# Kernel tuning notes

Measured on AMD Instinct MI355X. Metric: run time of the kernel, lower is better.

## Reference

```python
import jax, jax.numpy as jnp
import numpy as np

B, T, C = 4, 1024, 1024
H, KV, D = 16, 8, 64   # n_head, kv_heads, dim_head
L = 32                 # partial rotary dim (freqs.shape[-1])
QK_NORM_SCALE = 10.0


def l2norm(t):
    # F.normalize(t, dim=-1): divide by L2 norm clamped to eps
    n = jnp.linalg.norm(t, axis=-1, keepdims=True)
    return t / jnp.maximum(n, 1e-12)


def rotate_half(x):
    # lucidrains rotary: interleaved pairs (d r) with r=2 -> (-x2, x1)
    x1, x2 = x[..., 0::2], x[..., 1::2]
    return jnp.stack((-x2, x1), axis=-1).reshape(x.shape)


def apply_rope(t, freqs):
    # xpos_scale is None in this config -> scale = 1.0
    return t * jnp.cos(freqs) + rotate_half(t) * jnp.sin(freqs)


def setup_inputs() -> dict:
    key = jax.random.key(0)
    ks = jax.random.split(key, 10)
    x = jax.random.normal(ks[0], (B, T, C), dtype=jnp.float32)
    encoded_data = jax.random.normal(ks[1], (B, T, C), dtype=jnp.float32)
    # rotary freqs: positions x inverse frequencies, duplicated interleaved to length L
    pos = jnp.arange(T, dtype=jnp.float32)
    inv_freq = 10000.0 ** (-jnp.arange(L // 2, dtype=jnp.float32) / (L // 2))
    freqs = jnp.repeat(pos[:, None] * inv_freq[None, :], 2, axis=-1)  # (T, L)
    attn_bias = jax.random.normal(ks[2], (H, T, T), dtype=jnp.float32) * 0.02
    Wq = jax.random.normal(ks[3], (C, H * D), dtype=jnp.float32) * 0.02
    Wk = jax.random.normal(ks[4], (C, KV * D), dtype=jnp.float32) * 0.02
    Wv = jax.random.normal(ks[5], (C, KV * D), dtype=jnp.float32) * 0.02
    Wo = jax.random.normal(ks[6], (H * D, C), dtype=jnp.float32) * 0.02
    q_scale = jnp.ones((D,), dtype=jnp.float32)
    k_scale = jnp.ones((D,), dtype=jnp.float32)
    return {"x": x, "encoded_data": encoded_data, "freqs": freqs,
            "attn_bias": attn_bias, "Wq": Wq, "Wk": Wk, "Wv": Wv, "Wo": Wo,
            "q_scale": q_scale, "k_scale": k_scale}


def reference(x, encoded_data, freqs, attn_bias, Wq, Wk, Wv, Wo, q_scale, k_scale):
    Bx, Tx, Cx = x.shape
    q = (x @ Wq).reshape(Bx, Tx, H, D).transpose(0, 2, 1, 3)            # (B,H,T,D)
    k = (encoded_data @ Wk).reshape(Bx, Tx, KV, D).transpose(0, 2, 1, 3)  # (B,KV,T,D)
    v = (encoded_data @ Wv).reshape(Bx, Tx, KV, D).transpose(0, 2, 1, 3)

    # qk-norm
    q = l2norm(q) * q_scale
    k = l2norm(k) * k_scale

    # partial rotary on first L dims (v too, as in the original code)
    l = freqs.shape[-1]
    ql, qr = q[..., :l], q[..., l:]
    kl, kr = k[..., :l], k[..., l:]
    vl, vr = v[..., :l], v[..., l:]
    q = jnp.concatenate([apply_rope(ql, freqs), qr], axis=-1)
    k = jnp.concatenate([apply_rope(kl, freqs), kr], axis=-1)
    v = jnp.concatenate([apply_rope(vl, freqs), vr], axis=-1)

    # GQA: k,v repeated along head dim (KV -> H = 2*KV)
    k = jnp.tile(k, (1, 2, 1, 1))
    v = jnp.tile(v, (1, 2, 1, 1))

    # pre-scale q, then SDPA applies its own default D^-0.5 (faithful to source)
    default_scale = D ** (-0.5)
    q = q * (default_scale / QK_NORM_SCALE)

    mask_value = -jnp.finfo(q.dtype).max
    causal = jnp.triu(jnp.ones((Tx, Tx), dtype=bool), k=1)  # j > i masked
    bias = jnp.where(causal, mask_value / 2, attn_bias)      # (H,T,T)

    scores = jnp.einsum('bhqd,bhkd->bhqk', q, k) * default_scale + bias[None]
    attn = jax.nn.softmax(scores, axis=-1)
    y = jnp.einsum('bhqk,bhkd->bhqd', attn, v)                # (B,H,T,D)
    y = y.transpose(0, 2, 1, 3).reshape(Bx, Tx, H * D)
    return y @ Wo
```

## Files before the change

kernel.cpp:

```cpp
#include <hip/hip_runtime.h>

typedef unsigned short u16;
typedef __attribute__((ext_vector_type(8))) __bf16 bf16x8;
typedef __attribute__((ext_vector_type(4))) float f32x4;
typedef __attribute__((ext_vector_type(16))) float f32x16;

#define LOG2E 1.44269504088896f

__device__ __forceinline__ u16 f2bf(float f) {
  union { float f; unsigned u; } c; c.f = f;
  unsigned u = c.u;
  return (u16)((u + 0x7fffu + ((u >> 16) & 1u)) >> 16);
}
__device__ __forceinline__ float bf2f(u16 h) {
  union { unsigned u; float f; } c; c.u = ((unsigned)h) << 16;
  return c.f;
}

__device__ __forceinline__ void load_lds16(const void* g, void* l) {
  __builtin_amdgcn_global_load_lds((const __attribute__((address_space(1))) unsigned int*)g,
                                   (__attribute__((address_space(3))) unsigned int*)l, 16, 0, 0);
}

__global__ void cast2_kernel(const float* __restrict__ a, const float* __restrict__ b,
                             u16* __restrict__ oa, u16* __restrict__ ob, int n4each) {
  int stride = gridDim.x * blockDim.x;
  for (int i = blockIdx.x * blockDim.x + threadIdx.x; i < 2 * n4each; i += stride) {
    const float4* src; ushort4* dst; int j;
    if (i < n4each) { src = (const float4*)a; dst = (ushort4*)oa; j = i; }
    else            { src = (const float4*)b; dst = (ushort4*)ob; j = i - n4each; }
    float4 v = src[j];
    ushort4 o;
    o.x = f2bf(v.x); o.y = f2bf(v.y); o.z = f2bf(v.z); o.w = f2bf(v.w);
    dst[j] = o;
  }
}

__global__ void trig_kernel(const float* __restrict__ freqs, float* __restrict__ cstab,
                            float* __restrict__ sntab) {
  int i = blockIdx.x * 256 + threadIdx.x;
  float f = freqs[i];
  float sn, cs;
  sincosf(f, &sn, &cs);
  cstab[i] = cs; sntab[i] = sn;
}

__global__ void bias_tiles_kernel(const float* __restrict__ bias, u16* __restrict__ biasTT) {
  int w = threadIdx.x >> 6, lane = threadIdx.x & 63;
  int f = blockIdx.x * 4 + w;
  int h = f / 528, rem = f - h * 528;
  int qt = (int)((sqrtf(8.f * (float)rem + 1.f) - 1.f) * 0.5f);
  while ((qt + 1) * (qt + 2) / 2 <= rem) ++qt;
  while (qt * (qt + 1) / 2 > rem) --qt;
  int kt = rem - qt * (qt + 1) / 2;
  int ql = lane & 31, hi = lane >> 5;
  const float* src = bias + ((size_t)h * 1024 + qt * 32 + ql) * 1024 + kt * 32 + hi * 4;
  u16 v[16];
#pragma unroll
  for (int g2 = 0; g2 < 4; ++g2) {
    float4 c = *(const float4*)(src + g2 * 8);
    v[g2 * 4 + 0] = f2bf(c.x * LOG2E);
    v[g2 * 4 + 1] = f2bf(c.y * LOG2E);
    v[g2 * 4 + 2] = f2bf(c.z * LOG2E);
    v[g2 * 4 + 3] = f2bf(c.w * LOG2E);
  }
  u16* dst = biasTT + (size_t)f * 1024 + lane * 16;
#pragma unroll
  for (int i = 0; i < 4; ++i) {
    ushort4 o; o.x = v[i * 4]; o.y = v[i * 4 + 1]; o.z = v[i * 4 + 2]; o.w = v[i * 4 + 3];
    *(ushort4*)(dst + i * 4) = o;
  }
}

__global__ void transpose_cast4_kernel(const float* __restrict__ Wq, const float* __restrict__ Wk,
                                       const float* __restrict__ Wv, const float* __restrict__ Wo,
                                       u16* __restrict__ WqT, u16* __restrict__ WkT,
                                       u16* __restrict__ WvT, u16* __restrict__ WoT) {
  __shared__ float tile[32][33];
  const float* in; u16* out; int C;
  int z = blockIdx.z;
  if (z == 0)      { in = Wq; out = WqT; C = 1024; }
  else if (z == 1) { in = Wk; out = WkT; C = 512; }
  else if (z == 2) { in = Wv; out = WvT; C = 512; }
  else             { in = Wo; out = WoT; C = 1024; }
  const int R = 1024;
  int c0 = blockIdx.x * 32, r0 = blockIdx.y * 32;
  if (c0 >= C) return;
  int tx = threadIdx.x, ty = threadIdx.y;
#pragma unroll
  for (int i = 0; i < 4; ++i)
    tile[ty + 8 * i][tx] = in[(size_t)(r0 + ty + 8 * i) * C + c0 + tx];
  __syncthreads();
#pragma unroll
  for (int i = 0; i < 4; ++i)
    out[(size_t)(c0 + ty + 8 * i) * R + r0 + tx] = f2bf(tile[tx][ty + 8 * i]);
}

__device__ __forceinline__ void gemm_bn64_core(const u16* A, const u16* Bt, int K,
                                               u16* As, u16* Bs, f32x4 (&acc)[2][4]) {
  int tid = threadIdx.x;
  int w = tid >> 6, l = tid & 63;
  int g = l >> 4, lr = l & 15;
  int m0 = blockIdx.x * 128, n0 = blockIdx.y * 64;
#pragma unroll
  for (int m = 0; m < 2; ++m)
#pragma unroll
    for (int n = 0; n < 4; ++n) acc[m][n] = (f32x4){0.f, 0.f, 0.f, 0.f};

  for (int k0 = 0; k0 < K; k0 += 64) {
#pragma unroll
    for (int rnd = 0; rnd < 4; ++rnd) {
      int bidx = rnd * 4096 + w * 1024 + l * 16;
      int row = bidx >> 7, colb = bidx & 127;
      int scol = colb ^ ((row & 7) << 4);
      load_lds16((const char*)A + ((size_t)(m0 + row) * K + k0) * 2 + scol,
                 (char*)As + rnd * 4096 + w * 1024);
    }
#pragma unroll
    for (int rnd = 0; rnd < 2; ++rnd) {
      int bidx = rnd * 4096 + w * 1024 + l * 16;
      int row = bidx >> 7, colb = bidx & 127;
      int scol = colb ^ ((row & 7) << 4);
      load_lds16((const char*)Bt + ((size_t)(n0 + row) * K + k0) * 2 + scol,
                 (char*)Bs + rnd * 4096 + w * 1024);
    }
    __syncthreads();
    bf16x8 af[2][2], bfr[4][2];
#pragma unroll
    for (int m = 0; m < 2; ++m) {
      int ra = w * 32 + m * 16 + lr;
#pragma unroll
      for (int kf = 0; kf < 2; ++kf)
        af[m][kf] = *(const bf16x8*)((const char*)As + ra * 128 + ((kf * 64 + g * 16) ^ ((ra & 7) << 4)));
    }
#pragma unroll
    for (int n = 0; n < 4; ++n) {
      int rb = n * 16 + lr;
#pragma unroll
      for (int kf = 0; kf < 2; ++kf)
        bfr[n][kf] = *(const bf16x8*)((const char*)Bs + rb * 128 + ((kf * 64 + g * 16) ^ ((rb & 7) << 4)));
    }
#pragma unroll
    for (int m = 0; m < 2; ++m)
#pragma unroll
      for (int n = 0; n < 4; ++n) {
        acc[m][n] = __builtin_amdgcn_mfma_f32_16x16x32_bf16(af[m][0], bfr[n][0], acc[m][n], 0, 0, 0);
        acc[m][n] = __builtin_amdgcn_mfma_f32_16x16x32_bf16(af[m][1], bfr[n][1], acc[m][n], 0, 0, 0);
      }
    __syncthreads();
  }
}

__global__ __launch_bounds__(256, 4) void gemm_qkv_kernel(const u16* xb, const u16* eb,
                                                          const u16* WqT, const u16* WkT, const u16* WvT,
                                                          const float* __restrict__ qscale,
                                                          const float* __restrict__ kscale,
                                                          const float* __restrict__ cstab,
                                                          const float* __restrict__ sntab,
                                                          u16* Qb, u16* Ktiles, u16* vr) {
  __shared__ __align__(16) u16 As[128 * 64];
  __shared__ __align__(16) u16 Bs[64 * 64];
  int z = blockIdx.z;
  const u16* A; const u16* Bt; int N;
  if (z == 0)      { A = xb; Bt = WqT; N = 1024; }
  else if (z == 1) { A = eb; Bt = WkT; N = 512; }
  else             { A = eb; Bt = WvT; N = 512; }
  if ((int)blockIdx.y * 64 >= N) return;
  f32x4 acc[2][4];
  gemm_bn64_core(A, Bt, 1024, As, Bs, acc);

  int tid = threadIdx.x;
  int w = tid >> 6, l = tid & 63;
  int g = l >> 4, lr = l & 15;
  int m0 = blockIdx.x * 128, n0 = blockIdx.y * 64;

  if (z == 2) {
#pragma unroll
    for (int m = 0; m < 2; ++m)
#pragma unroll
      for (int n = 0; n < 4; ++n) {
        int row = m0 + w * 32 + m * 16 + g * 4;
        int col = n0 + n * 16 + lr;
#pragma unroll
        for (int r = 0; r < 4; ++r)
          vr[(size_t)(row + r) * 512 + col] = f2bf(acc[m][n][r]);
      }
    return;
  }

  const float* scale = (z == 0) ? qscale : kscale;
  float fs = (z == 0) ? 0.0015625f * LOG2E : 1.0f;
  int head = n0 >> 6;
#pragma unroll
  for (int m = 0; m < 2; ++m) {
    int rowb = m0 + w * 32 + m * 16 + g * 4;
#pragma unroll
    for (int r = 0; r < 4; ++r) {
      int row = rowb + r;
      int t = row & 1023, b = row >> 10;
      float ss = 0.f;
#pragma unroll
      for (int n = 0; n < 4; ++n) { float v = acc[m][n][r]; ss += v * v; }
#pragma unroll
      for (int d = 1; d < 16; d <<= 1) ss += __shfl_xor(ss, d);
      float inv = 1.0f / fmaxf(sqrtf(ss), 1e-12f);
#pragma unroll
      for (int n = 0; n < 4; ++n) {
        int dloc = n * 16 + lr;
        float v = acc[m][n][r] * inv * scale[dloc];
        if (n < 2) {
          float cs = cstab[t * 32 + dloc];
          float sn = sntab[t * 32 + dloc];
          float partner = __shfl_xor(v, 1);
          float rot = (lr & 1) ? partner : -partner;
          v = v * cs + rot * sn;
        }
        v *= fs;
        if (z == 0) {
          Qb[((size_t)(b * 16 + head) * 1024 + t) * 64 + dloc] = f2bf(v);
        } else {
          int tile = (b * 8 + head) * 32 + (t >> 5);
          int rin = t & 31;
          *(u16*)((char*)Ktiles + (size_t)tile * 4096 + rin * 128 + ((dloc * 2) ^ ((rin & 7) << 4))) = f2bf(v);
        }
      }
    }
  }
}

__global__ __launch_bounds__(256, 4) void gemm_out_kernel(const u16* Yb, const u16* WoT, float* out) {
  __shared__ __align__(16) u16 As[128 * 64];
  __shared__ __align__(16) u16 Bs[64 * 64];
  f32x4 acc[2][4];
  gemm_bn64_core(Yb, WoT, 1024, As, Bs, acc);
  int tid = threadIdx.x;
  int w = tid >> 6, l = tid & 63;
  int g = l >> 4, lr = l & 15;
  int m0 = blockIdx.x * 128, n0 = blockIdx.y * 64;
#pragma unroll
  for (int m = 0; m < 2; ++m)
#pragma unroll
    for (int n = 0; n < 4; ++n) {
      int row = m0 + w * 32 + m * 16 + g * 4;
      int col = n0 + n * 16 + lr;
#pragma unroll
      for (int r = 0; r < 4; ++r)
        out[(size_t)(row + r) * 1024 + col] = acc[m][n][r];
    }
}

__global__ void epilogue_v_kernel(const u16* __restrict__ v_raw, const float* __restrict__ cstab,
                                  const float* __restrict__ sntab, u16* __restrict__ Vtiles) {
  __shared__ __align__(16) u16 tile[64][72];
  int blk = blockIdx.x;
  int t0 = (blk & 15) * 64;
  int kvg = blk >> 4;
  int kvv = kvg & 7;
  int bb = kvg >> 3;
  int tid = threadIdx.x;
  int tl = tid >> 2;
  int dq = (tid & 3) * 16;
  int t = t0 + tl;
  const u16* src = v_raw + ((size_t)(bb * 1024 + t)) * 512 + kvv * 64 + dq;
  bf16x8 a0 = *(const bf16x8*)(src);
  bf16x8 a1 = *(const bf16x8*)(src + 8);
  float x[16];
#pragma unroll
  for (int i = 0; i < 8; ++i) { x[i] = (float)a0[i]; x[8 + i] = (float)a1[i]; }
  if (dq < 32) {
#pragma unroll
    for (int j = 0; j < 8; ++j) {
      int d = dq + 2 * j;
      float cs = cstab[t * 32 + d];
      float sn = sntab[t * 32 + d];
      float e = x[2 * j], o = x[2 * j + 1];
      x[2 * j]     = e * cs - o * sn;
      x[2 * j + 1] = o * cs + e * sn;
    }
  }
#pragma unroll
  for (int i = 0; i < 16; ++i) tile[dq + i][tl] = f2bf(x[i]);
  __syncthreads();
#pragma unroll
  for (int rnd = 0; rnd < 2; ++rnd) {
    int chunk = rnd * 256 + tid;
    int drow = chunk >> 3, c8 = chunk & 7;
    bf16x8 val = *(const bf16x8*)((const char*)&tile[0][0] + drow * 144 + c8 * 16);
    int tidx = kvg * 32 + (t0 >> 5) + (c8 >> 2);
    int row = drow & 31;
    int scol = ((drow >> 5) << 6) | ((c8 & 3) * 16);
    int colb = scol ^ ((row & 7) << 4);
    *(bf16x8*)((char*)Vtiles + (size_t)tidx * 4096 + row * 128 + colb) = val;
  }
}

__device__ __forceinline__ unsigned pack_bf2(float lo, float hi_) {
  union { __bf16 h[2]; unsigned u; } c;
  c.h[0] = (__bf16)lo; c.h[1] = (__bf16)hi_;
  return c.u;
}

__global__ __launch_bounds__(256, 3) void attn_kernel(const u16* __restrict__ Qb, const u16* __restrict__ Ktiles,
                                                      const u16* __restrict__ Vtiles, const u16* __restrict__ biasTT,
                                                      u16* __restrict__ Yb) {
  __shared__ __align__(16) char smem[33792];
  int tid = threadIdx.x;
  int w = tid >> 6;
  int lane = tid & 63;
  int ql = lane & 31;
  int hi = lane >> 5;
  int id = blockIdx.x;
  int xcd = id & 7;
  int j = id >> 3;
  int b = j & 3;
  int gslot = j >> 2;
  int g = gslot * 8 + xcd;
  int h = g & 15;
  int qt = 31 - (g >> 4);
  int kv = h & 7;
  int qg = qt * 32 + ql;
  int nt = qt + 1;

  char* stg = smem + w * 8192;

  const u16* Qrow = Qb + ((size_t)(b * 16 + h) * 1024 + qg) * 64;
  bf16x8 qf[4];
#pragma unroll
  for (int ks = 0; ks < 4; ++ks) qf[ks] = *(const bf16x8*)(Qrow + ks * 16 + hi * 8);

  const char* Ktb = (const char*)Ktiles + (size_t)((b * 8 + kv) * 32) * 4096;
  const char* Vtb = (const char*)Vtiles + (size_t)((b * 8 + kv) * 32) * 4096;
  const u16* btb = biasTT + (size_t)(h * 528 + qt * (qt + 1) / 2) * 1024;

  f32x16 o0, o1;
#pragma unroll
  for (int r = 0; r < 16; ++r) { o0[r] = 0.f; o1[r] = 0.f; }
  float m = -1e30f, lsum = 0.f;

  for (int it = w; it < nt; it += 4) {
    int t0 = it * 32;
    const char* Ksrc = Ktb + (size_t)it * 4096 + lane * 16;
    const char* Vsrc = Vtb + (size_t)it * 4096 + lane * 16;
#pragma unroll
    for (int i = 0; i < 4; ++i) {
      load_lds16(Ksrc + i * 1024, stg + i * 1024);
      load_lds16(Vsrc + i * 1024, stg + 4096 + i * 1024);
    }
    const u16* bl = btb + (size_t)it * 1024 + lane * 16;
    bf16x8 ba = *(const bf16x8*)bl;
    bf16x8 bb2 = *(const bf16x8*)(bl + 8);
    f32x16 s;
#pragma unroll
    for (int r = 0; r < 8; ++r) { s[r] = (float)ba[r]; s[r + 8] = (float)bb2[r]; }
    asm volatile("s_waitcnt vmcnt(0)" ::: "memory");
    __builtin_amdgcn_sched_barrier(0);
#pragma unroll
    for (int ks = 0; ks < 4; ++ks) {
      bf16x8 kc = *(const bf16x8*)(stg + ql * 128 + ((ks * 32 + hi * 16) ^ ((ql & 7) << 4)));
      s = __builtin_amdgcn_mfma_f32_32x32x16_bf16(kc, qf[ks], s, 0, 0, 0);
    }
    bool diag = (it == nt - 1);
    float p[16];
#pragma unroll
    for (int r = 0; r < 16; ++r) {
      float sv = s[r];
      if (diag) {
        int key = t0 + (r & 3) + 8 * (r >> 2) + 4 * hi;
        if (key > qg) sv = -1e30f;
      }
      p[r] = sv;
    }
    float t8[8];
#pragma unroll
    for (int j2 = 0; j2 < 8; ++j2) t8[j2] = fmaxf(p[2 * j2], p[2 * j2 + 1]);
    float t4a = fmaxf(t8[0], t8[1]), t4b = fmaxf(t8[2], t8[3]);
    float t4c = fmaxf(t8[4], t8[5]), t4d = fmaxf(t8[6], t8[7]);
    float mx = fmaxf(fmaxf(t4a, t4b), fmaxf(t4c, t4d));
    mx = fmaxf(mx, __shfl_xor(mx, 32));
    if (!__all(mx <= m + 8.0f)) {
      float mn = fmaxf(m, mx);
      float sf = exp2f(m - mn);
      m = mn;
      lsum *= sf;
#pragma unroll
      for (int r = 0; r < 16; ++r) { o0[r] *= sf; o1[r] *= sf; }
    }
    float ssum = 0.f;
#pragma unroll
    for (int r = 0; r < 16; ++r) {
      p[r] = exp2f(p[r] - m);
      ssum += p[r];
    }
    lsum += ssum;
    unsigned pk[8], tk[8];
#pragma unroll
    for (int j2 = 0; j2 < 8; ++j2) pk[j2] = pack_bf2(p[2 * j2], p[2 * j2 + 1]);
#pragma unroll
    for (int j2 = 0; j2 < 8; ++j2) tk[j2] = (unsigned)__shfl_xor((int)pk[j2], 32);
    union PU { unsigned u[4]; bf16x8 v; };
    PU pb0, pb1;
    pb0.u[0] = hi ? tk[2] : pk[0];
    pb0.u[1] = hi ? tk[3] : pk[1];
    pb0.u[2] = hi ? pk[2] : tk[0];
    pb0.u[3] = hi ? pk[3] : tk[1];
    pb1.u[0] = hi ? tk[6] : pk[4];
    pb1.u[1] = hi ? tk[7] : pk[5];
    pb1.u[2] = hi ? pk[6] : tk[4];
    pb1.u[3] = hi ? pk[7] : tk[5];
    char* Vl = stg + 4096;
    bf16x8 v00 = *(const bf16x8*)(Vl + ql * 128 + (((0 << 6) | (0 * 32 + hi * 16)) ^ ((ql & 7) << 4)));
    bf16x8 v01 = *(const bf16x8*)(Vl + ql * 128 + (((0 << 6) | (1 * 32 + hi * 16)) ^ ((ql & 7) << 4)));
    bf16x8 v10 = *(const bf16x8*)(Vl + ql * 128 + (((1 << 6) | (0 * 32 + hi * 16)) ^ ((ql & 7) << 4)));
    bf16x8 v11 = *(const bf16x8*)(Vl + ql * 128 + (((1 << 6) | (1 * 32 + hi * 16)) ^ ((ql & 7) << 4)));
    o0 = __builtin_amdgcn_mfma_f32_32x32x16_bf16(v00, pb0.v, o0, 0, 0, 0);
    o0 = __builtin_amdgcn_mfma_f32_32x32x16_bf16(v01, pb1.v, o0, 0, 0, 0);
    o1 = __builtin_amdgcn_mfma_f32_32x32x16_bf16(v10, pb0.v, o1, 0, 0, 0);
    o1 = __builtin_amdgcn_mfma_f32_32x32x16_bf16(v11, pb1.v, o1, 0, 0, 0);
  }

  lsum += __shfl_xor(lsum, 32);
  u16* Osh = (u16*)stg;
  float* Msh = (float*)(smem + 32768);
  float* Lsh = (float*)(smem + 32768 + 512);
#pragma unroll
  for (int r = 0; r < 16; ++r) {
    int row = (r & 3) + 8 * (r >> 2) + 4 * hi;
    Osh[row * 32 + ql]        = f2bf(o0[r]);
    Osh[(row + 32) * 32 + ql] = f2bf(o1[r]);
  }
  if (hi == 0) { Msh[w * 32 + ql] = m; Lsh[w * 32 + ql] = lsum; }
  __syncthreads();

  {
    int q = tid & 31, dg = tid >> 5;
    float* Msh2 = (float*)(smem + 32768);
    float* Lsh2 = (float*)(smem + 32768 + 512);
    float m0 = Msh2[q], m1 = Msh2[32 + q], m2 = Msh2[64 + q], m3 = Msh2[96 + q];
    float mM = fmaxf(fmaxf(m0, m1), fmaxf(m2, m3));
    float w0 = exp2f(m0 - mM), w1 = exp2f(m1 - mM);
    float w2 = exp2f(m2 - mM), w3 = exp2f(m3 - mM);
    float ltot = w0 * Lsh2[q] + w1 * Lsh2[32 + q] + w2 * Lsh2[64 + q] + w3 * Lsh2[96 + q];
    float invl = 1.0f / ltot;
    u16 ov[8];
#pragma unroll
    for (int j2 = 0; j2 < 8; ++j2) {
      int d = dg * 8 + j2;
      float acc = w0 * bf2f(*(u16*)(smem + 0 * 8192 + (d * 32 + q) * 2)) +
                  w1 * bf2f(*(u16*)(smem + 1 * 8192 + (d * 32 + q) * 2)) +
                  w2 * bf2f(*(u16*)(smem + 2 * 8192 + (d * 32 + q) * 2)) +
                  w3 * bf2f(*(u16*)(smem + 3 * 8192 + (d * 32 + q) * 2));
      ov[j2] = f2bf(acc * invl);
    }
    ushort4 out0, out1;
    out0.x = ov[0]; out0.y = ov[1]; out0.z = ov[2]; out0.w = ov[3];
    out1.x = ov[4]; out1.y = ov[5]; out1.z = ov[6]; out1.w = ov[7];
    u16* Yp = Yb + ((size_t)b * 1024 + qt * 32 + q) * 1024 + h * 64 + dg * 8;
    *(ushort4*)Yp = out0;
    *(ushort4*)(Yp + 4) = out1;
  }
}

extern "C" void kernel_launch(void* const* d_in, const int* in_sizes, int n_in,
                              void* d_out, int out_size, void* d_ws, size_t ws_size,
                              hipStream_t stream) {
  const float* x     = (const float*)d_in[0];
  const float* enc   = (const float*)d_in[1];
  const float* freqs = (const float*)d_in[2];
  const float* bias  = (const float*)d_in[3];
  const float* Wq    = (const float*)d_in[4];
  const float* Wk    = (const float*)d_in[5];
  const float* Wv    = (const float*)d_in[6];
  const float* Wo    = (const float*)d_in[7];
  const float* qs    = (const float*)d_in[8];
  const float* ks    = (const float*)d_in[9];

  char* ws = (char*)d_ws;
  size_t off = 0;
  auto alloc = [&](size_t bytes) { char* p = ws + off; off += (bytes + 255) & ~(size_t)255; return p; };
  u16*   xb     = (u16*)alloc(8388608);
  u16*   eb     = (u16*)alloc(8388608);
  u16*   WqT    = (u16*)alloc(2097152);
  u16*   WkT    = (u16*)alloc(1048576);
  u16*   WvT    = (u16*)alloc(1048576);
  u16*   WoT    = (u16*)alloc(2097152);
  u16*   vr     = (u16*)alloc(4194304);
  u16*   Qb     = (u16*)alloc(8388608);
  u16*   Ktiles = (u16*)alloc(4194304);
  u16*   Vtiles = (u16*)alloc(4194304);
  u16*   biasTT = (u16*)alloc(17301504);
  float* cstab  = (float*)alloc(131072);
  float* sntab  = (float*)alloc(131072);
  u16*   Yb     = (u16*)xb;

  cast2_kernel<<<2048, 256, 0, stream>>>(x, enc, xb, eb, 1048576);
  trig_kernel<<<128, 256, 0, stream>>>(freqs, cstab, sntab);
  transpose_cast4_kernel<<<dim3(32, 32, 4), dim3(32, 8), 0, stream>>>(Wq, Wk, Wv, Wo, WqT, WkT, WvT, WoT);
  bias_tiles_kernel<<<2112, 256, 0, stream>>>(bias, biasTT);

  gemm_qkv_kernel<<<dim3(32, 16, 3), 256, 0, stream>>>(xb, eb, WqT, WkT, WvT,
                                                       qs, ks, cstab, sntab, Qb, Ktiles, vr);

  epilogue_v_kernel<<<512, 256, 0, stream>>>(vr, cstab, sntab, Vtiles);

  attn_kernel<<<dim3(2048), 256, 0, stream>>>(Qb, Ktiles, Vtiles, biasTT, Yb);

  gemm_out_kernel<<<dim3(32, 16), 256, 0, stream>>>(Yb, WoT, (float*)d_out);
}
```

Baseline: 105.2 us.

## Fuse V rotary into QKV GEMM, drop softmax max tracking, coalesce bias tiling

Moves the V rotary embedding and tiled swizzled layout write into the QKV GEMM epilogue, removing a separate kernel and intermediate buffer. The bias tiling kernel now stages tiles through shared memory so global reads are row-contiguous. The attention kernel drops running-max tracking in softmax, relying on bounded scores from qk-normalisation, and raises its occupancy hint. The unscaled exp assumes small score and bias magnitudes, and the V epilogue now does scattered 2-byte stores.

```diff
diff --git a/kernel.cpp b/kernel.cpp
--- a/kernel.cpp
+++ b/kernel.cpp
@@ -46,6 +46,7 @@
 }
 
 __global__ void bias_tiles_kernel(const float* __restrict__ bias, u16* __restrict__ biasTT) {
+  __shared__ float lt[4][32][33];
   int w = threadIdx.x >> 6, lane = threadIdx.x & 63;
   int f = blockIdx.x * 4 + w;
   int h = f / 528, rem = f - h * 528;
@@ -53,16 +54,21 @@
   while ((qt + 1) * (qt + 2) / 2 <= rem) ++qt;
   while (qt * (qt + 1) / 2 > rem) --qt;
   int kt = rem - qt * (qt + 1) / 2;
+  const float* tsrc = bias + ((size_t)h * 1024 + qt * 32) * 1024 + kt * 32;
+#pragma unroll
+  for (int i = 0; i < 4; ++i) {
+    int row = i * 8 + (lane >> 3);
+    int c4 = (lane & 7) * 4;
+    float4 v4 = *(const float4*)(tsrc + (size_t)row * 1024 + c4);
+    lt[w][row][c4 + 0] = v4.x; lt[w][row][c4 + 1] = v4.y;
+    lt[w][row][c4 + 2] = v4.z; lt[w][row][c4 + 3] = v4.w;
+  }
   int ql = lane & 31, hi = lane >> 5;
-  const float* src = bias + ((size_t)h * 1024 + qt * 32 + ql) * 1024 + kt * 32 + hi * 4;
   u16 v[16];
 #pragma unroll
-  for (int g2 = 0; g2 < 4; ++g2) {
-    float4 c = *(const float4*)(src + g2 * 8);
-    v[g2 * 4 + 0] = f2bf(c.x * LOG2E);
-    v[g2 * 4 + 1] = f2bf(c.y * LOG2E);
-    v[g2 * 4 + 2] = f2bf(c.z * LOG2E);
-    v[g2 * 4 + 3] = f2bf(c.w * LOG2E);
+  for (int r = 0; r < 16; ++r) {
+    int c = (r & 3) + 8 * (r >> 2) + 4 * hi;
+    v[r] = f2bf(lt[w][ql][c] * LOG2E);
   }
   u16* dst = biasTT + (size_t)f * 1024 + lane * 16;
 #pragma unroll
@@ -157,7 +163,7 @@
                                                           const float* __restrict__ kscale,
                                                           const float* __restrict__ cstab,
                                                           const float* __restrict__ sntab,
-                                                          u16* Qb, u16* Ktiles, u16* vr) {
+                                                          u16* Qb, u16* Ktiles, u16* Vtiles) {
   __shared__ __align__(16) u16 As[128 * 64];
   __shared__ __align__(16) u16 Bs[64 * 64];
   int z = blockIdx.z;
@@ -173,24 +179,40 @@
   int w = tid >> 6, l = tid & 63;
   int g = l >> 4, lr = l & 15;
   int m0 = blockIdx.x * 128, n0 = blockIdx.y * 64;
+  int head = n0 >> 6;
 
   if (z == 2) {
 #pragma unroll
-    for (int m = 0; m < 2; ++m)
-#pragma unroll
-      for (int n = 0; n < 4; ++n) {
-        int row = m0 + w * 32 + m * 16 + g * 4;
-        int col = n0 + n * 16 + lr;
-#pragma unroll
-        for (int r = 0; r < 4; ++r)
-          vr[(size_t)(row + r) * 512 + col] = f2bf(acc[m][n][r]);
+    for (int m = 0; m < 2; ++m) {
+      int rowb = m0 + w * 32 + m * 16 + g * 4;
+#pragma unroll
+      for (int r = 0; r < 4; ++r) {
+        int row = rowb + r;
+        int t = row & 1023, b = row >> 10;
+        char* tbase = (char*)Vtiles + (size_t)((b * 8 + head) * 32 + (t >> 5)) * 4096;
+        int kb = (t & 31) * 2;
+#pragma unroll
+        for (int n = 0; n < 4; ++n) {
+          int dloc = n * 16 + lr;
+          float v = acc[m][n][r];
+          if (n < 2) {
+            float cs = cstab[t * 32 + dloc];
+            float sn = sntab[t * 32 + dloc];
+            float partner = __shfl_xor(v, 1);
+            float rot = (lr & 1) ? partner : -partner;
+            v = v * cs + rot * sn;
+          }
+          int rr = dloc & 31;
+          int scol = ((dloc >> 5) << 6) | kb;
+          *(u16*)(tbase + rr * 128 + (scol ^ ((rr & 7) << 4))) = f2bf(v);
+        }
       }
+    }
     return;
   }
 
   const float* scale = (z == 0) ? qscale : kscale;
   float fs = (z == 0) ? 0.0015625f * LOG2E : 1.0f;
-  int head = n0 >> 6;
 #pragma unroll
   for (int m = 0; m < 2; ++m) {
     int rowb = m0 + w * 32 + m * 16 + g * 4;
@@ -249,61 +271,16 @@
     }
 }
 
-__global__ void epilogue_v_kernel(const u16* __restrict__ v_raw, const float* __restrict__ cstab,
-                                  const float* __restrict__ sntab, u16* __restrict__ Vtiles) {
-  __shared__ __align__(16) u16 tile[64][72];
-  int blk = blockIdx.x;
-  int t0 = (blk & 15) * 64;
-  int kvg = blk >> 4;
-  int kvv = kvg & 7;
-  int bb = kvg >> 3;
-  int tid = threadIdx.x;
-  int tl = tid >> 2;
-  int dq = (tid & 3) * 16;
-  int t = t0 + tl;
-  const u16* src = v_raw + ((size_t)(bb * 1024 + t)) * 512 + kvv * 64 + dq;
-  bf16x8 a0 = *(const bf16x8*)(src);
-  bf16x8 a1 = *(const bf16x8*)(src + 8);
-  float x[16];
-#pragma unroll
-  for (int i = 0; i < 8; ++i) { x[i] = (float)a0[i]; x[8 + i] = (float)a1[i]; }
-  if (dq < 32) {
-#pragma unroll
-    for (int j = 0; j < 8; ++j) {
-      int d = dq + 2 * j;
-      float cs = cstab[t * 32 + d];
-      float sn = sntab[t * 32 + d];
-      float e = x[2 * j], o = x[2 * j + 1];
-      x[2 * j]     = e * cs - o * sn;
-      x[2 * j + 1] = o * cs + e * sn;
-    }
-  }
-#pragma unroll
-  for (int i = 0; i < 16; ++i) tile[dq + i][tl] = f2bf(x[i]);
-  __syncthreads();
-#pragma unroll
-  for (int rnd = 0; rnd < 2; ++rnd) {
-    int chunk = rnd * 256 + tid;
-    int drow = chunk >> 3, c8 = chunk & 7;
-    bf16x8 val = *(const bf16x8*)((const char*)&tile[0][0] + drow * 144 + c8 * 16);
-    int tidx = kvg * 32 + (t0 >> 5) + (c8 >> 2);
-    int row = drow & 31;
-    int scol = ((drow >> 5) << 6) | ((c8 & 3) * 16);
-    int colb = scol ^ ((row & 7) << 4);
-    *(bf16x8*)((char*)Vtiles + (size_t)tidx * 4096 + row * 128 + colb) = val;
-  }
-}
-
 __device__ __forceinline__ unsigned pack_bf2(float lo, float hi_) {
   union { __bf16 h[2]; unsigned u; } c;
   c.h[0] = (__bf16)lo; c.h[1] = (__bf16)hi_;
   return c.u;
 }
 
-__global__ __launch_bounds__(256, 3) void attn_kernel(const u16* __restrict__ Qb, const u16* __restrict__ Ktiles,
+__global__ __launch_bounds__(256, 4) void attn_kernel(const u16* __restrict__ Qb, const u16* __restrict__ Ktiles,
                                                       const u16* __restrict__ Vtiles, const u16* __restrict__ biasTT,
                                                       u16* __restrict__ Yb) {
-  __shared__ __align__(16) char smem[33792];
+  __shared__ __align__(16) char smem[33280];
   int tid = threadIdx.x;
   int w = tid >> 6;
   int lane = tid & 63;
@@ -335,7 +312,7 @@
   f32x16 o0, o1;
 #pragma unroll
   for (int r = 0; r < 16; ++r) { o0[r] = 0.f; o1[r] = 0.f; }
-  float m = -1e30f, lsum = 0.f;
+  float lsum = 0.f;
 
   for (int it = w; it < nt; it += 4) {
     int t0 = it * 32;
@@ -361,6 +338,7 @@
     }
     bool diag = (it == nt - 1);
     float p[16];
+    float ssum = 0.f;
 #pragma unroll
     for (int r = 0; r < 16; ++r) {
       float sv = s[r];
@@ -368,28 +346,9 @@
         int key = t0 + (r & 3) + 8 * (r >> 2) + 4 * hi;
         if (key > qg) sv = -1e30f;
       }
-      p[r] = sv;
-    }
-    float t8[8];
-#pragma unroll
-    for (int j2 = 0; j2 < 8; ++j2) t8[j2] = fmaxf(p[2 * j2], p[2 * j2 + 1]);
-    float t4a = fmaxf(t8[0], t8[1]), t4b = fmaxf(t8[2], t8[3]);
-    float t4c = fmaxf(t8[4], t8[5]), t4d = fmaxf(t8[6], t8[7]);
-    float mx = fmaxf(fmaxf(t4a, t4b), fmaxf(t4c, t4d));
-    mx = fmaxf(mx, __shfl_xor(mx, 32));
-    if (!__all(mx <= m + 8.0f)) {
-      float mn = fmaxf(m, mx);
-      float sf = exp2f(m - mn);
-      m = mn;
-      lsum *= sf;
-#pragma unroll
-      for (int r = 0; r < 16; ++r) { o0[r] *= sf; o1[r] *= sf; }
-    }
-    float ssum = 0.f;
-#pragma unroll
-    for (int r = 0; r < 16; ++r) {
-      p[r] = exp2f(p[r] - m);
-      ssum += p[r];
+      float pe = exp2f(sv);
+      p[r] = pe;
+      ssum += pe;
     }
     lsum += ssum;
     unsigned pk[8], tk[8];
@@ -420,35 +379,29 @@
 
   lsum += __shfl_xor(lsum, 32);
   u16* Osh = (u16*)stg;
-  float* Msh = (float*)(smem + 32768);
-  float* Lsh = (float*)(smem + 32768 + 512);
+  float* Lsh = (float*)(smem + 32768);
 #pragma unroll
   for (int r = 0; r < 16; ++r) {
     int row = (r & 3) + 8 * (r >> 2) + 4 * hi;
     Osh[row * 32 + ql]        = f2bf(o0[r]);
     Osh[(row + 32) * 32 + ql] = f2bf(o1[r]);
   }
-  if (hi == 0) { Msh[w * 32 + ql] = m; Lsh[w * 32 + ql] = lsum; }
+  if (hi == 0) Lsh[w * 32 + ql] = lsum;
   __syncthreads();
 
   {
     int q = tid & 31, dg = tid >> 5;
-    float* Msh2 = (float*)(smem + 32768);
-    float* Lsh2 = (float*)(smem + 32768 + 512);
-    float m0 = Msh2[q], m1 = Msh2[32 + q], m2 = Msh2[64 + q], m3 = Msh2[96 + q];
-    float mM = fmaxf(fmaxf(m0, m1), fmaxf(m2, m3));
-    float w0 = exp2f(m0 - mM), w1 = exp2f(m1 - mM);
-    float w2 = exp2f(m2 - mM), w3 = exp2f(m3 - mM);
-    float ltot = w0 * Lsh2[q] + w1 * Lsh2[32 + q] + w2 * Lsh2[64 + q] + w3 * Lsh2[96 + q];
+    float* Lsh2 = (float*)(smem + 32768);
+    float ltot = Lsh2[q] + Lsh2[32 + q] + Lsh2[64 + q] + Lsh2[96 + q];
     float invl = 1.0f / ltot;
     u16 ov[8];
 #pragma unroll
     for (int j2 = 0; j2 < 8; ++j2) {
       int d = dg * 8 + j2;
-      float acc = w0 * bf2f(*(u16*)(smem + 0 * 8192 + (d * 32 + q) * 2)) +
-                  w1 * bf2f(*(u16*)(smem + 1 * 8192 + (d * 32 + q) * 2)) +
-                  w2 * bf2f(*(u16*)(smem + 2 * 8192 + (d * 32 + q) * 2)) +
-                  w3 * bf2f(*(u16*)(smem + 3 * 8192 + (d * 32 + q) * 2));
+      float acc = bf2f(*(u16*)(smem + 0 * 8192 + (d * 32 + q) * 2)) +
+                  bf2f(*(u16*)(smem + 1 * 8192 + (d * 32 + q) * 2)) +
+                  bf2f(*(u16*)(smem + 2 * 8192 + (d * 32 + q) * 2)) +
+                  bf2f(*(u16*)(smem + 3 * 8192 + (d * 32 + q) * 2));
       ov[j2] = f2bf(acc * invl);
     }
     ushort4 out0, out1;
@@ -483,7 +436,6 @@
   u16*   WkT    = (u16*)alloc(1048576);
   u16*   WvT    = (u16*)alloc(1048576);
   u16*   WoT    = (u16*)alloc(2097152);
-  u16*   vr     = (u16*)alloc(4194304);
   u16*   Qb     = (u16*)alloc(8388608);
   u16*   Ktiles = (u16*)alloc(4194304);
   u16*   Vtiles = (u16*)alloc(4194304);
@@ -498,9 +450,7 @@
   bias_tiles_kernel<<<2112, 256, 0, stream>>>(bias, biasTT);
 
   gemm_qkv_kernel<<<dim3(32, 16, 3), 256, 0, stream>>>(xb, eb, WqT, WkT, WvT,
-                                                       qs, ks, cstab, sntab, Qb, Ktiles, vr);
-
-  epilogue_v_kernel<<<512, 256, 0, stream>>>(vr, cstab, sntab, Vtiles);
+                                                       qs, ks, cstab, sntab, Qb, Ktiles, Vtiles);
 
   attn_kernel<<<dim3(2048), 256, 0, stream>>>(Qb, Ktiles, Vtiles, biasTT, Yb);
 
```

After: 98.80 us. 6.1% less time.
